# Kernel optimization log

Measured on AMD Instinct MI355X. Metric: run time of the kernel, lower is better.

Reference implementation:

```python
import jax, jax.numpy as jnp
import numpy as np

B, D, H = 32768, 256, 8
DH = D // H
SCALE = 1.0 / float(np.sqrt(DH))
# neighbor indices: for query node i, context = the other 3 nodes (in order)
NEIGH = np.array([[1, 2, 3], [0, 2, 3], [0, 1, 3], [0, 1, 2]], dtype=np.int32)


def setup_inputs() -> dict:
    key = jax.random.key(0)
    ks = jax.random.split(key, 6)
    s = 0.02
    mk = lambda k: jax.random.normal(k, (D, D), jnp.float32) * s
    return {
        "tokens": jax.random.normal(ks[0], (B, 4, D), jnp.float32),
        "Wq": mk(ks[1]),
        "Wk": mk(ks[2]),
        "Wv": mk(ks[3]),
        "Wr": mk(ks[4]),
        "Wo": mk(ks[5]),
        "ln_g": jnp.ones((D,), jnp.float32),
        "ln_b": jnp.zeros((D,), jnp.float32),
    }


def reference(tokens, Wq, Wk, Wv, Wr, Wo, ln_g, ln_b):
    # tokens: [B,4,D]. All 4 modality queries share one GCA block (share_gca=True),
    # so we batch the 4-node complete-graph message passing into one pass.
    neigh = jnp.asarray(NEIGH)
    ctx = tokens[:, neigh]                    # [B,4,3,D]
    Q = tokens @ Wq.T                         # [B,4,D]
    K = ctx @ Wk.T                            # [B,4,3,D]
    V = ctx @ Wv.T
    R = ctx @ Wr.T
    V_eff = jax.nn.sigmoid(R) * V             # gated values
    Qh = Q.reshape(B, 4, H, DH)
    Kh = K.reshape(B, 4, 3, H, DH)
    Vh = V_eff.reshape(B, 4, 3, H, DH)
    scores = jnp.einsum('bihd,bilhd->bihl', Qh, Kh) * SCALE   # [B,4,H,3]
    attn = jax.nn.softmax(scores, axis=-1)    # dropout = identity (eval mode)
    out = jnp.einsum('bihl,bilhd->bihd', attn, Vh).reshape(B, 4, D)
    out = out @ Wo.T
    y = tokens + out                          # residual
    mu = y.mean(-1, keepdims=True)
    var = y.var(-1, keepdims=True)
    y = (y - mu) / jnp.sqrt(var + 1e-5) * ln_g + ln_b   # LayerNorm
    # attn: [B,4,H,3] -> per-query attn maps (attn[:, i] == attn for modality-i query, [B,H,1,3] squeezed)
    return y, attn
```

## Files before the change

### kernel.cpp

```cpp
#include <hip/hip_runtime.h>
#include <stdint.h>


#define D_DIM   256
#define H_NUM   8
#define RT      64
#define NTHR    512
#define ROWS_TOT 131072
#define Y_SZ    33554432
#define SCALE_F 0.17677669529663687f
#define W_ELEMS 65536
#define WS_NEED (5 * W_ELEMS * 2)

#define SX_LD   264
#define AO_LD   264
#define SP_LD   20

typedef __attribute__((ext_vector_type(8))) short bf16x8;
typedef __attribute__((ext_vector_type(4))) float f32x4;

__device__ __forceinline__ float b2f(uint16_t s) {
    union { uint32_t u; float f; } c; c.u = ((uint32_t)s) << 16; return c.f;
}
__device__ __forceinline__ uint16_t f2b(float f) {
    union { float f; uint32_t u; } c; c.f = f;
    return (uint16_t)((c.u + 0x7fffu + ((c.u >> 16) & 1u)) >> 16);
}
__device__ __forceinline__ bf16x8 cvt8(const float* p) {
    const float4 a = *(const float4*)p;
    const float4 b = *(const float4*)(p + 4);
    bf16x8 r;
    r[0] = (short)f2b(a.x); r[1] = (short)f2b(a.y);
    r[2] = (short)f2b(a.z); r[3] = (short)f2b(a.w);
    r[4] = (short)f2b(b.x); r[5] = (short)f2b(b.y);
    r[6] = (short)f2b(b.z); r[7] = (short)f2b(b.w);
    return r;
}
__device__ __forceinline__ uint2 pack4(f32x4 a) {
    uint2 p;
    p.x = (uint32_t)f2b(a[0]) | ((uint32_t)f2b(a[1]) << 16);
    p.y = (uint32_t)f2b(a[2]) | ((uint32_t)f2b(a[3]) << 16);
    return p;
}

__global__ __launch_bounds__(256)
void conv_weights(const float* __restrict__ Wq, const float* __restrict__ Wk,
                  const float* __restrict__ Wv, const float* __restrict__ Wr,
                  const float* __restrict__ Wo, uint16_t* __restrict__ dst)
{
    const int m = blockIdx.x >> 6;
    const float* src = (m == 0) ? Wq : (m == 1) ? Wk : (m == 2) ? Wv
                     : (m == 3) ? Wr : Wo;
    const int base = (blockIdx.x & 63) * 1024 + threadIdx.x * 4;
    const float4 v = *(const float4*)&src[base];
    uint2 pk;
    pk.x = (uint32_t)f2b(v.x) | ((uint32_t)f2b(v.y) << 16);
    pk.y = (uint32_t)f2b(v.z) | ((uint32_t)f2b(v.w) << 16);
    *(uint2*)&dst[(size_t)m * W_ELEMS + base] = pk;
}

template<bool WBF16>
__global__ __launch_bounds__(NTHR, 4)
void cmaa_fused(const float* __restrict__ tok,
                const float* __restrict__ Wq, const float* __restrict__ Wk,
                const float* __restrict__ Wv, const float* __restrict__ Wr,
                const float* __restrict__ Wo,
                const uint16_t* __restrict__ wbf,
                const float* __restrict__ lng, const float* __restrict__ lnb,
                float* __restrict__ outp)
{
    __shared__ __align__(16) uint16_t sX [RT * SX_LD];
    __shared__ __align__(16) uint16_t sAO[RT * AO_LD];
    __shared__ __align__(16) uint16_t sAL[RT * H_NUM * 4];
    __shared__ __align__(16) float    sPT[RT * SP_LD];

    const int tid  = threadIdx.x;
    const int wv   = tid >> 6;
    const int lane = tid & 63;
    const int l15  = lane & 15;
    const int quad = lane >> 4;
    const int R0   = blockIdx.x * RT;

    {
        const float* g = tok + (size_t)R0 * D_DIM;
        #pragma unroll
        for (int it = 0; it < 4; ++it) {
            const int t = tid + it * NTHR;
            const int row = t >> 5, c = t & 31;
            *(bf16x8*)&sX[row * SX_LD + c * 8] = cvt8(&g[row * D_DIM + c * 8]);
        }
    }
    __syncthreads();

    const bool qk = (wv < 4);
    const int  hl = wv & 3;

    #pragma unroll
    for (int p = 0; p < 2; ++p) {
        const int h = p * 4 + hl;
        const int colbase = h * 32;
        const float*    WF0 = qk ? Wq : Wv;
        const float*    WF1 = qk ? Wk : Wr;
        const uint16_t* WB0 = wbf + (size_t)(qk ? 0 : 2) * W_ELEMS;
        const uint16_t* WB1 = WB0 + W_ELEMS;

        f32x4 acc[2][2][4];
        #pragma unroll
        for (int m = 0; m < 2; ++m)
            #pragma unroll
            for (int ct = 0; ct < 2; ++ct)
                #pragma unroll
                for (int nt = 0; nt < 4; ++nt)
                    acc[m][ct][nt] = (f32x4){0.f, 0.f, 0.f, 0.f};

        #pragma unroll
        for (int kk = 0; kk < 8; ++kk) {
            const int k0 = kk * 32;
            bf16x8 ax[4];
            #pragma unroll
            for (int nt = 0; nt < 4; ++nt)
                ax[nt] = *(const bf16x8*)&sX[(nt * 16 + l15) * SX_LD + k0 + quad * 8];
            bf16x8 b0[2], b1[2];
            #pragma unroll
            for (int ct = 0; ct < 2; ++ct) {
                const int wrow = colbase + ct * 16 + l15;
                if constexpr (WBF16) {
                    b0[ct] = *(const bf16x8*)&WB0[(size_t)wrow * D_DIM + k0 + quad * 8];
                    b1[ct] = *(const bf16x8*)&WB1[(size_t)wrow * D_DIM + k0 + quad * 8];
                } else {
                    b0[ct] = cvt8(&WF0[(size_t)wrow * D_DIM + k0 + quad * 8]);
                    b1[ct] = cvt8(&WF1[(size_t)wrow * D_DIM + k0 + quad * 8]);
                }
            }
            #pragma unroll
            for (int ct = 0; ct < 2; ++ct)
                #pragma unroll
                for (int nt = 0; nt < 4; ++nt)
                    acc[0][ct][nt] = __builtin_amdgcn_mfma_f32_16x16x32_bf16(b0[ct], ax[nt], acc[0][ct][nt], 0, 0, 0);
            #pragma unroll
            for (int ct = 0; ct < 2; ++ct)
                #pragma unroll
                for (int nt = 0; nt < 4; ++nt)
                    acc[1][ct][nt] = __builtin_amdgcn_mfma_f32_16x16x32_bf16(b1[ct], ax[nt], acc[1][ct][nt], 0, 0, 0);
        }

        if (qk) {
            #pragma unroll
            for (int nt = 0; nt < 4; ++nt) {
                float sc[3];
                #pragma unroll
                for (int m = 1; m <= 3; ++m) {
                    float s = 0.f;
                    #pragma unroll
                    for (int ct = 0; ct < 2; ++ct)
                        #pragma unroll
                        for (int r = 0; r < 4; ++r)
                            s += acc[0][ct][nt][r] * __shfl_xor(acc[1][ct][nt][r], m);
                    s += __shfl_xor(s, 16);
                    s += __shfl_xor(s, 32);
                    sc[m - 1] = s * SCALE_F;
                }
                const float mx = fmaxf(sc[0], fmaxf(sc[1], sc[2]));
                const float e1 = __expf(sc[0] - mx), e2 = __expf(sc[1] - mx), e3 = __expf(sc[2] - mx);
                const float inv = 1.f / (e1 + e2 + e3);
                const float a1 = e1 * inv, a2 = e2 * inv, a3 = e3 * inv;
                const int token = nt * 16 + l15;
                if (quad == 0) {
                    ushort4 aw;
                    aw.x = 0; aw.y = f2b(a1); aw.z = f2b(a2); aw.w = f2b(a3);
                    *(ushort4*)&sAL[(token * H_NUM + h) * 4] = aw;
                    const int ii = token & 3;
                    float* ap = outp + Y_SZ + ((size_t)(R0 + token) * H_NUM + h) * 3;
                    #pragma unroll
                    for (int l = 0; l < 3; ++l) {
                        const int jj = l + (l >= ii);
                        const int m  = ii ^ jj;
                        ap[l] = (m == 1) ? a1 : ((m == 2) ? a2 : a3);
                    }
                }
            }
        } else {
            #pragma unroll
            for (int ct = 0; ct < 2; ++ct)
                #pragma unroll
                for (int nt = 0; nt < 4; ++nt)
                    #pragma unroll
                    for (int r = 0; r < 4; ++r)
                        acc[0][ct][nt][r] *= 1.f / (1.f + __expf(-acc[1][ct][nt][r]));
        }
        __syncthreads();

        if (!qk) {
            #pragma unroll
            for (int nt = 0; nt < 4; ++nt) {
                const int token = nt * 16 + l15;
                const ushort4 aw = *(const ushort4*)&sAL[(token * H_NUM + h) * 4];
                const float a1 = b2f(aw.y), a2 = b2f(aw.z), a3 = b2f(aw.w);
                #pragma unroll
                for (int ct = 0; ct < 2; ++ct) {
                    f32x4 ao;
                    #pragma unroll
                    for (int r = 0; r < 4; ++r) {
                        const float v = acc[0][ct][nt][r];
                        ao[r] = a1 * __shfl_xor(v, 1)
                              + a2 * __shfl_xor(v, 2)
                              + a3 * __shfl_xor(v, 3);
                    }
                    *(uint2*)&sAO[token * AO_LD + colbase + ct * 16 + quad * 4] = pack4(ao);
                }
            }
        }
        __syncthreads();
    }

    const uint16_t* WoB = wbf + (size_t)4 * W_ELEMS;
    f32x4 acc3[2][4];
    #pragma unroll
    for (int ct = 0; ct < 2; ++ct)
        #pragma unroll
        for (int nt = 0; nt < 4; ++nt)
            acc3[ct][nt] = (f32x4){0.f, 0.f, 0.f, 0.f};

    #pragma unroll
    for (int kk = 0; kk < 8; ++kk) {
        const int k0 = kk * 32;
        bf16x8 ao[4];
        #pragma unroll
        for (int nt = 0; nt < 4; ++nt)
            ao[nt] = *(const bf16x8*)&sAO[(nt * 16 + l15) * AO_LD + k0 + quad * 8];
        bf16x8 bw[2];
        #pragma unroll
        for (int ct = 0; ct < 2; ++ct) {
            const int wrow = wv * 32 + ct * 16 + l15;
            if constexpr (WBF16)
                bw[ct] = *(const bf16x8*)&WoB[(size_t)wrow * D_DIM + k0 + quad * 8];
            else
                bw[ct] = cvt8(&Wo[(size_t)wrow * D_DIM + k0 + quad * 8]);
        }
        #pragma unroll
        for (int ct = 0; ct < 2; ++ct)
            #pragma unroll
            for (int nt = 0; nt < 4; ++nt)
                acc3[ct][nt] = __builtin_amdgcn_mfma_f32_16x16x32_bf16(bw[ct], ao[nt], acc3[ct][nt], 0, 0, 0);
    }

    #pragma unroll
    for (int nt = 0; nt < 4; ++nt) {
        const int token = nt * 16 + l15;
        float s1 = 0.f, s2 = 0.f;
        #pragma unroll
        for (int ct = 0; ct < 2; ++ct) {
            const ushort4 xv = *(const ushort4*)&sX[token * SX_LD + wv * 32 + ct * 16 + quad * 4];
            const float x0 = b2f(xv.x), x1 = b2f(xv.y), x2 = b2f(xv.z), x3 = b2f(xv.w);
            acc3[ct][nt][0] += x0; acc3[ct][nt][1] += x1;
            acc3[ct][nt][2] += x2; acc3[ct][nt][3] += x3;
            #pragma unroll
            for (int r = 0; r < 4; ++r) {
                const float y = acc3[ct][nt][r];
                s1 += y; s2 += y * y;
            }
        }
        s1 += __shfl_xor(s1, 16); s1 += __shfl_xor(s1, 32);
        s2 += __shfl_xor(s2, 16); s2 += __shfl_xor(s2, 32);
        if (quad == 0) {
            float2 ps; ps.x = s1; ps.y = s2;
            *(float2*)&sPT[token * SP_LD + wv * 2] = ps;
        }
    }
    __syncthreads();

    #pragma unroll
    for (int nt = 0; nt < 4; ++nt) {
        const int token = nt * 16 + l15;
        const f32x4* pp = (const f32x4*)&sPT[token * SP_LD];
        const f32x4 q0 = pp[0], q1 = pp[1], q2 = pp[2], q3 = pp[3];
        const float s1 = q0[0] + q0[2] + q1[0] + q1[2] + q2[0] + q2[2] + q3[0] + q3[2];
        const float s2 = q0[1] + q0[3] + q1[1] + q1[3] + q2[1] + q2[3] + q3[1] + q3[3];
        const float mean = s1 * (1.f / 256.f);
        const float var  = fmaxf(s2 * (1.f / 256.f) - mean * mean, 0.f);
        const float rstd = rsqrtf(var + 1e-5f);
        float* orow = outp + (size_t)(R0 + token) * D_DIM;
        #pragma unroll
        for (int ct = 0; ct < 2; ++ct) {
            const int c0 = wv * 32 + ct * 16 + quad * 4;
            const float4 g4 = *(const float4*)&lng[c0];
            const float4 b4 = *(const float4*)&lnb[c0];
            float4 o4;
            o4.x = (acc3[ct][nt][0] - mean) * rstd * g4.x + b4.x;
            o4.y = (acc3[ct][nt][1] - mean) * rstd * g4.y + b4.y;
            o4.z = (acc3[ct][nt][2] - mean) * rstd * g4.z + b4.z;
            o4.w = (acc3[ct][nt][3] - mean) * rstd * g4.w + b4.w;
            *(float4*)&orow[c0] = o4;
        }
    }
}

extern "C" void kernel_launch(void* const* d_in, const int* in_sizes, int n_in,
                              void* d_out, int out_size, void* d_ws, size_t ws_size,
                              hipStream_t stream) {
    (void)in_sizes; (void)n_in; (void)out_size;
    const float* tok = (const float*)d_in[0];
    const float* Wq  = (const float*)d_in[1];
    const float* Wk  = (const float*)d_in[2];
    const float* Wv  = (const float*)d_in[3];
    const float* Wr  = (const float*)d_in[4];
    const float* Wo  = (const float*)d_in[5];
    const float* lng = (const float*)d_in[6];
    const float* lnb = (const float*)d_in[7];
    float* outp = (float*)d_out;
    uint16_t* wbf = (uint16_t*)d_ws;

    dim3 grid(ROWS_TOT / RT), block(NTHR);
    if (ws_size >= (size_t)WS_NEED) {
        conv_weights<<<dim3(320), dim3(256), 0, stream>>>(Wq, Wk, Wv, Wr, Wo, wbf);
        cmaa_fused<true><<<grid, block, 0, stream>>>(
            tok, Wq, Wk, Wv, Wr, Wo, wbf, lng, lnb, outp);
    } else {
        cmaa_fused<false><<<grid, block, 0, stream>>>(
            tok, Wq, Wk, Wv, Wr, Wo, wbf, lng, lnb, outp);
    }
}
```

Baseline: 429.5 us.

## Preload weights into registers and stage attention maps in LDS for coalesced store

All weight fragments for each projection pass are loaded into registers before the MFMA loop, and the Wo fragments are prefetched during the second pass so their latency overlaps with the softmax and gating work. The attention probabilities are now kept in fp32 in shared memory in output order and written out as one coalesced float4 store per block, replacing scattered 4-byte global writes. The launch bound is lowered from 4 to 2 blocks per SM so the larger register footprint fits, which cuts occupancy.

```diff
diff --git a/kernel.cpp b/kernel.cpp
--- a/kernel.cpp
+++ b/kernel.cpp
@@ -60,7 +60,7 @@
 }
 
 template<bool WBF16>
-__global__ __launch_bounds__(NTHR, 4)
+__global__ __launch_bounds__(NTHR, 2)
 void cmaa_fused(const float* __restrict__ tok,
                 const float* __restrict__ Wq, const float* __restrict__ Wk,
                 const float* __restrict__ Wv, const float* __restrict__ Wr,
@@ -69,10 +69,10 @@
                 const float* __restrict__ lng, const float* __restrict__ lnb,
                 float* __restrict__ outp)
 {
-    __shared__ __align__(16) uint16_t sX [RT * SX_LD];
-    __shared__ __align__(16) uint16_t sAO[RT * AO_LD];
-    __shared__ __align__(16) uint16_t sAL[RT * H_NUM * 4];
-    __shared__ __align__(16) float    sPT[RT * SP_LD];
+    __shared__ __align__(16) uint16_t sX  [RT * SX_LD];
+    __shared__ __align__(16) uint16_t sAO [RT * AO_LD];
+    __shared__ __align__(16) float    sALf[RT * H_NUM * 3];
+    __shared__ __align__(16) float    sPT [RT * SP_LD];
 
     const int tid  = threadIdx.x;
     const int wv   = tid >> 6;
@@ -94,6 +94,8 @@
 
     const bool qk = (wv < 4);
     const int  hl = wv & 3;
+
+    bf16x8 wo_reg[2][8];
 
     #pragma unroll
     for (int p = 0; p < 2; ++p) {
@@ -104,6 +106,22 @@
         const uint16_t* WB0 = wbf + (size_t)(qk ? 0 : 2) * W_ELEMS;
         const uint16_t* WB1 = WB0 + W_ELEMS;
 
+        bf16x8 w0[2][8], w1[2][8];
+        #pragma unroll
+        for (int ct = 0; ct < 2; ++ct) {
+            const int wrow = colbase + ct * 16 + l15;
+            #pragma unroll
+            for (int kk = 0; kk < 8; ++kk) {
+                if constexpr (WBF16) {
+                    w0[ct][kk] = *(const bf16x8*)&WB0[(size_t)wrow * D_DIM + kk * 32 + quad * 8];
+                    w1[ct][kk] = *(const bf16x8*)&WB1[(size_t)wrow * D_DIM + kk * 32 + quad * 8];
+                } else {
+                    w0[ct][kk] = cvt8(&WF0[(size_t)wrow * D_DIM + kk * 32 + quad * 8]);
+                    w1[ct][kk] = cvt8(&WF1[(size_t)wrow * D_DIM + kk * 32 + quad * 8]);
+                }
+            }
+        }
+
         f32x4 acc[2][2][4];
         #pragma unroll
         for (int m = 0; m < 2; ++m)
@@ -120,28 +138,31 @@
             #pragma unroll
             for (int nt = 0; nt < 4; ++nt)
                 ax[nt] = *(const bf16x8*)&sX[(nt * 16 + l15) * SX_LD + k0 + quad * 8];
-            bf16x8 b0[2], b1[2];
+            #pragma unroll
+            for (int ct = 0; ct < 2; ++ct)
+                #pragma unroll
+                for (int nt = 0; nt < 4; ++nt)
+                    acc[0][ct][nt] = __builtin_amdgcn_mfma_f32_16x16x32_bf16(w0[ct][kk], ax[nt], acc[0][ct][nt], 0, 0, 0);
+            #pragma unroll
+            for (int ct = 0; ct < 2; ++ct)
+                #pragma unroll
+                for (int nt = 0; nt < 4; ++nt)
+                    acc[1][ct][nt] = __builtin_amdgcn_mfma_f32_16x16x32_bf16(w1[ct][kk], ax[nt], acc[1][ct][nt], 0, 0, 0);
+        }
+
+        if (p == 1) {
+            const uint16_t* WoB = wbf + (size_t)4 * W_ELEMS;
             #pragma unroll
             for (int ct = 0; ct < 2; ++ct) {
-                const int wrow = colbase + ct * 16 + l15;
-                if constexpr (WBF16) {
-                    b0[ct] = *(const bf16x8*)&WB0[(size_t)wrow * D_DIM + k0 + quad * 8];
-                    b1[ct] = *(const bf16x8*)&WB1[(size_t)wrow * D_DIM + k0 + quad * 8];
-                } else {
-                    b0[ct] = cvt8(&WF0[(size_t)wrow * D_DIM + k0 + quad * 8]);
-                    b1[ct] = cvt8(&WF1[(size_t)wrow * D_DIM + k0 + quad * 8]);
-                }
-            }
-            #pragma unroll
-            for (int ct = 0; ct < 2; ++ct)
-                #pragma unroll
-                for (int nt = 0; nt < 4; ++nt)
-                    acc[0][ct][nt] = __builtin_amdgcn_mfma_f32_16x16x32_bf16(b0[ct], ax[nt], acc[0][ct][nt], 0, 0, 0);
-            #pragma unroll
-            for (int ct = 0; ct < 2; ++ct)
-                #pragma unroll
-                for (int nt = 0; nt < 4; ++nt)
-                    acc[1][ct][nt] = __builtin_amdgcn_mfma_f32_16x16x32_bf16(b1[ct], ax[nt], acc[1][ct][nt], 0, 0, 0);
+                const int wrow = wv * 32 + ct * 16 + l15;
+                #pragma unroll
+                for (int kk = 0; kk < 8; ++kk) {
+                    if constexpr (WBF16)
+                        wo_reg[ct][kk] = *(const bf16x8*)&WoB[(size_t)wrow * D_DIM + kk * 32 + quad * 8];
+                    else
+                        wo_reg[ct][kk] = cvt8(&Wo[(size_t)wrow * D_DIM + kk * 32 + quad * 8]);
+                }
+            }
         }
 
         if (qk) {
@@ -163,19 +184,16 @@
                 const float mx = fmaxf(sc[0], fmaxf(sc[1], sc[2]));
                 const float e1 = __expf(sc[0] - mx), e2 = __expf(sc[1] - mx), e3 = __expf(sc[2] - mx);
                 const float inv = 1.f / (e1 + e2 + e3);
-                const float a1 = e1 * inv, a2 = e2 * inv, a3 = e3 * inv;
+                const float am[3] = { e1 * inv, e2 * inv, e3 * inv };
                 const int token = nt * 16 + l15;
                 if (quad == 0) {
-                    ushort4 aw;
-                    aw.x = 0; aw.y = f2b(a1); aw.z = f2b(a2); aw.w = f2b(a3);
-                    *(ushort4*)&sAL[(token * H_NUM + h) * 4] = aw;
                     const int ii = token & 3;
-                    float* ap = outp + Y_SZ + ((size_t)(R0 + token) * H_NUM + h) * 3;
+                    float* al = &sALf[(token * H_NUM + h) * 3];
                     #pragma unroll
                     for (int l = 0; l < 3; ++l) {
                         const int jj = l + (l >= ii);
                         const int m  = ii ^ jj;
-                        ap[l] = (m == 1) ? a1 : ((m == 2) ? a2 : a3);
+                        al[l] = am[m - 1];
                     }
                 }
             }
@@ -194,17 +212,24 @@
             #pragma unroll
             for (int nt = 0; nt < 4; ++nt) {
                 const int token = nt * 16 + l15;
-                const ushort4 aw = *(const ushort4*)&sAL[(token * H_NUM + h) * 4];
-                const float a1 = b2f(aw.y), a2 = b2f(aw.z), a3 = b2f(aw.w);
+                const int ii = token & 3;
+                const float* al = &sALf[(token * H_NUM + h) * 3];
+                float am[3];
+                #pragma unroll
+                for (int m = 1; m <= 3; ++m) {
+                    const int jj = ii ^ m;
+                    const int l  = jj - (jj > ii ? 1 : 0);
+                    am[m - 1] = al[l];
+                }
                 #pragma unroll
                 for (int ct = 0; ct < 2; ++ct) {
                     f32x4 ao;
                     #pragma unroll
                     for (int r = 0; r < 4; ++r) {
                         const float v = acc[0][ct][nt][r];
-                        ao[r] = a1 * __shfl_xor(v, 1)
-                              + a2 * __shfl_xor(v, 2)
-                              + a3 * __shfl_xor(v, 3);
+                        ao[r] = am[0] * __shfl_xor(v, 1)
+                              + am[1] * __shfl_xor(v, 2)
+                              + am[2] * __shfl_xor(v, 3);
                     }
                     *(uint2*)&sAO[token * AO_LD + colbase + ct * 16 + quad * 4] = pack4(ao);
                 }
@@ -213,7 +238,11 @@
         __syncthreads();
     }
 
-    const uint16_t* WoB = wbf + (size_t)4 * W_ELEMS;
+    if (tid < 384) {
+        const float4 v = *(const float4*)&sALf[tid * 4];
+        *(float4*)&outp[Y_SZ + (size_t)R0 * (H_NUM * 3) + tid * 4] = v;
+    }
+
     f32x4 acc3[2][4];
     #pragma unroll
     for (int ct = 0; ct < 2; ++ct)
@@ -228,20 +257,11 @@
         #pragma unroll
         for (int nt = 0; nt < 4; ++nt)
             ao[nt] = *(const bf16x8*)&sAO[(nt * 16 + l15) * AO_LD + k0 + quad * 8];
-        bf16x8 bw[2];
-        #pragma unroll
-        for (int ct = 0; ct < 2; ++ct) {
-            const int wrow = wv * 32 + ct * 16 + l15;
-            if constexpr (WBF16)
-                bw[ct] = *(const bf16x8*)&WoB[(size_t)wrow * D_DIM + k0 + quad * 8];
-            else
-                bw[ct] = cvt8(&Wo[(size_t)wrow * D_DIM + k0 + quad * 8]);
-        }
         #pragma unroll
         for (int ct = 0; ct < 2; ++ct)
             #pragma unroll
             for (int nt = 0; nt < 4; ++nt)
-                acc3[ct][nt] = __builtin_amdgcn_mfma_f32_16x16x32_bf16(bw[ct], ao[nt], acc3[ct][nt], 0, 0, 0);
+                acc3[ct][nt] = __builtin_amdgcn_mfma_f32_16x16x32_bf16(wo_reg[ct][kk], ao[nt], acc3[ct][nt], 0, 0, 0);
     }
 
     #pragma unroll
```

Result: slower. 452.1 us (+5.3%).

## Use 1024-thread blocks and MFMA for attention scores and weighted values

Applied to the files above, without the earlier changes.

Doubles the block to 16 waves so Q/K and V/R projections all run in one pass, one head per wave, instead of two passes over 8 waves. Q and K are staged to shared memory and the gated V is stored transposed. The per-token 4x4 score matrix and the attention-weighted sum of V are then computed with small MFMA ops instead of cross-lane shuffles. The attention maps are written out as coalesced float4 stores from shared memory. In exchange, shared memory per block and per-thread register pressure rise, occupancy may drop, and the small MFMAs are mostly zero-padded.

```diff
diff --git a/kernel.cpp b/kernel.cpp
--- a/kernel.cpp
+++ b/kernel.cpp
@@ -5,7 +5,7 @@
 #define D_DIM   256
 #define H_NUM   8
 #define RT      64
-#define NTHR    512
+#define NTHR    1024
 #define ROWS_TOT 131072
 #define Y_SZ    33554432
 #define SCALE_F 0.17677669529663687f
@@ -13,8 +13,9 @@
 #define WS_NEED (5 * W_ELEMS * 2)
 
 #define SX_LD   264
-#define AO_LD   264
-#define SP_LD   20
+#define QK_LD   264
+#define VT_LD   68
+#define SP_LD   36
 
 typedef __attribute__((ext_vector_type(8))) short bf16x8;
 typedef __attribute__((ext_vector_type(4))) float f32x4;
@@ -69,10 +70,13 @@
                 const float* __restrict__ lng, const float* __restrict__ lnb,
                 float* __restrict__ outp)
 {
-    __shared__ __align__(16) uint16_t sX [RT * SX_LD];
-    __shared__ __align__(16) uint16_t sAO[RT * AO_LD];
-    __shared__ __align__(16) uint16_t sAL[RT * H_NUM * 4];
-    __shared__ __align__(16) float    sPT[RT * SP_LD];
+    __shared__ __align__(16) uint16_t sX  [RT * SX_LD];
+    __shared__ __align__(16) uint16_t sQ  [RT * QK_LD];
+    __shared__ __align__(16) uint16_t sK  [RT * QK_LD];
+    __shared__ __align__(16) uint16_t sVT [D_DIM * VT_LD];
+    __shared__ __align__(16) float    sALf[RT * H_NUM * 3];
+    __shared__ __align__(16) uint2    sALpk[RT * H_NUM];
+    __shared__ __align__(16) float    sPT [RT * SP_LD];
 
     const int tid  = threadIdx.x;
     const int wv   = tid >> 6;
@@ -84,7 +88,7 @@
     {
         const float* g = tok + (size_t)R0 * D_DIM;
         #pragma unroll
-        for (int it = 0; it < 4; ++it) {
+        for (int it = 0; it < 2; ++it) {
             const int t = tid + it * NTHR;
             const int row = t >> 5, c = t & 31;
             *(bf16x8*)&sX[row * SX_LD + c * 8] = cvt8(&g[row * D_DIM + c * 8]);
@@ -92,16 +96,12 @@
     }
     __syncthreads();
 
-    const bool qk = (wv < 4);
-    const int  hl = wv & 3;
-
-    #pragma unroll
-    for (int p = 0; p < 2; ++p) {
-        const int h = p * 4 + hl;
-        const int colbase = h * 32;
-        const float*    WF0 = qk ? Wq : Wv;
-        const float*    WF1 = qk ? Wk : Wr;
-        const uint16_t* WB0 = wbf + (size_t)(qk ? 0 : 2) * W_ELEMS;
+    {
+        const bool qkw = (wv < 8);
+        const int  h   = wv & 7;
+        const float*    WF0 = qkw ? Wq : Wv;
+        const float*    WF1 = qkw ? Wk : Wr;
+        const uint16_t* WB0 = wbf + (size_t)(qkw ? 0 : 2) * W_ELEMS;
         const uint16_t* WB1 = WB0 + W_ELEMS;
 
         f32x4 acc[2][2][4];
@@ -123,7 +123,7 @@
             bf16x8 b0[2], b1[2];
             #pragma unroll
             for (int ct = 0; ct < 2; ++ct) {
-                const int wrow = colbase + ct * 16 + l15;
+                const int wrow = h * 32 + ct * 16 + l15;
                 if constexpr (WBF16) {
                     b0[ct] = *(const bf16x8*)&WB0[(size_t)wrow * D_DIM + k0 + quad * 8];
                     b1[ct] = *(const bf16x8*)&WB1[(size_t)wrow * D_DIM + k0 + quad * 8];
@@ -144,154 +144,172 @@
                     acc[1][ct][nt] = __builtin_amdgcn_mfma_f32_16x16x32_bf16(b1[ct], ax[nt], acc[1][ct][nt], 0, 0, 0);
         }
 
-        if (qk) {
-            #pragma unroll
-            for (int nt = 0; nt < 4; ++nt) {
-                float sc[3];
-                #pragma unroll
-                for (int m = 1; m <= 3; ++m) {
-                    float s = 0.f;
-                    #pragma unroll
-                    for (int ct = 0; ct < 2; ++ct)
-                        #pragma unroll
-                        for (int r = 0; r < 4; ++r)
-                            s += acc[0][ct][nt][r] * __shfl_xor(acc[1][ct][nt][r], m);
-                    s += __shfl_xor(s, 16);
-                    s += __shfl_xor(s, 32);
-                    sc[m - 1] = s * SCALE_F;
+        if (qkw) {
+            #pragma unroll
+            for (int ct = 0; ct < 2; ++ct)
+                #pragma unroll
+                for (int nt = 0; nt < 4; ++nt) {
+                    const int tk = nt * 16 + l15;
+                    const int dc = h * 32 + ct * 16 + quad * 4;
+                    *(uint2*)&sQ[tk * QK_LD + dc] = pack4(acc[0][ct][nt]);
+                    *(uint2*)&sK[tk * QK_LD + dc] = pack4(acc[1][ct][nt]);
                 }
-                const float mx = fmaxf(sc[0], fmaxf(sc[1], sc[2]));
-                const float e1 = __expf(sc[0] - mx), e2 = __expf(sc[1] - mx), e3 = __expf(sc[2] - mx);
-                const float inv = 1.f / (e1 + e2 + e3);
-                const float a1 = e1 * inv, a2 = e2 * inv, a3 = e3 * inv;
-                const int token = nt * 16 + l15;
-                if (quad == 0) {
-                    ushort4 aw;
-                    aw.x = 0; aw.y = f2b(a1); aw.z = f2b(a2); aw.w = f2b(a3);
-                    *(ushort4*)&sAL[(token * H_NUM + h) * 4] = aw;
-                    const int ii = token & 3;
-                    float* ap = outp + Y_SZ + ((size_t)(R0 + token) * H_NUM + h) * 3;
-                    #pragma unroll
-                    for (int l = 0; l < 3; ++l) {
-                        const int jj = l + (l >= ii);
-                        const int m  = ii ^ jj;
-                        ap[l] = (m == 1) ? a1 : ((m == 2) ? a2 : a3);
-                    }
-                }
-            }
         } else {
             #pragma unroll
             for (int ct = 0; ct < 2; ++ct)
                 #pragma unroll
                 for (int nt = 0; nt < 4; ++nt)
                     #pragma unroll
-                    for (int r = 0; r < 4; ++r)
-                        acc[0][ct][nt][r] *= 1.f / (1.f + __expf(-acc[1][ct][nt][r]));
-        }
-        __syncthreads();
-
-        if (!qk) {
-            #pragma unroll
-            for (int nt = 0; nt < 4; ++nt) {
-                const int token = nt * 16 + l15;
-                const ushort4 aw = *(const ushort4*)&sAL[(token * H_NUM + h) * 4];
-                const float a1 = b2f(aw.y), a2 = b2f(aw.z), a3 = b2f(aw.w);
-                #pragma unroll
-                for (int ct = 0; ct < 2; ++ct) {
-                    f32x4 ao;
-                    #pragma unroll
                     for (int r = 0; r < 4; ++r) {
-                        const float v = acc[0][ct][nt][r];
-                        ao[r] = a1 * __shfl_xor(v, 1)
-                              + a2 * __shfl_xor(v, 2)
-                              + a3 * __shfl_xor(v, 3);
+                        const float ve = acc[0][ct][nt][r] *
+                            (1.f / (1.f + __expf(-acc[1][ct][nt][r])));
+                        const int dd = h * 32 + ct * 16 + quad * 4 + r;
+                        sVT[dd * VT_LD + nt * 16 + l15] = f2b(ve);
                     }
-                    *(uint2*)&sAO[token * AO_LD + colbase + ct * 16 + quad * 4] = pack4(ao);
-                }
+        }
+    }
+    __syncthreads();
+
+    #pragma unroll
+    for (int uu = 0; uu < 2; ++uu) {
+        const int u  = wv + 16 * uu;
+        const int hh = u >> 2;
+        const int tt = u & 3;
+        const int tk = tt * 16 + l15;
+
+        const bf16x8 kf = *(const bf16x8*)&sK[tk * QK_LD + hh * 32 + quad * 8];
+        const bf16x8 qf = *(const bf16x8*)&sQ[tk * QK_LD + hh * 32 + quad * 8];
+        f32x4 sc = __builtin_amdgcn_mfma_f32_16x16x32_bf16(
+            kf, qf, (f32x4){0.f, 0.f, 0.f, 0.f}, 0, 0, 0);
+
+        if (quad == (l15 >> 2)) {
+            const int r0 = l15 & 3;
+            float sv[4], e[4];
+            #pragma unroll
+            for (int r = 0; r < 4; ++r) sv[r] = sc[r] * SCALE_F;
+            float mx = -1e30f;
+            #pragma unroll
+            for (int r = 0; r < 4; ++r) mx = fmaxf(mx, (r == r0) ? -1e30f : sv[r]);
+            float sum = 0.f;
+            #pragma unroll
+            for (int r = 0; r < 4; ++r) {
+                e[r] = (r == r0) ? 0.f : __expf(sv[r] - mx);
+                sum += e[r];
             }
-        }
-        __syncthreads();
-    }
-
-    const uint16_t* WoB = wbf + (size_t)4 * W_ELEMS;
-    f32x4 acc3[2][4];
+            const float inv = 1.f / sum;
+            float al[4];
+            #pragma unroll
+            for (int r = 0; r < 4; ++r) al[r] = e[r] * inv;
+            float* af = &sALf[(tk * H_NUM + hh) * 3];
+            #pragma unroll
+            for (int r = 0; r < 4; ++r)
+                if (r != r0) af[r - (r > r0 ? 1 : 0)] = al[r];
+            uint2 pk;
+            pk.x = (uint32_t)f2b(al[0]) | ((uint32_t)f2b(al[1]) << 16);
+            pk.y = (uint32_t)f2b(al[2]) | ((uint32_t)f2b(al[3]) << 16);
+            sALpk[tk * H_NUM + hh] = pk;
+        }
+
+        const uint2 apk = sALpk[tk * H_NUM + hh];
+        const bool qm = (quad == ((l15 >> 3) & 1));
+        const bool hi = (l15 & 4) != 0;
+        union { uint32_t u[4]; bf16x8 v; } A;
+        A.u[0] = (qm && !hi) ? apk.x : 0u;
+        A.u[1] = (qm && !hi) ? apk.y : 0u;
+        A.u[2] = (qm &&  hi) ? apk.x : 0u;
+        A.u[3] = (qm &&  hi) ? apk.y : 0u;
+
+        const bf16x8 vb0 = *(const bf16x8*)&sVT[(hh * 32 + l15) * VT_LD + tt * 16 + quad * 8];
+        const bf16x8 vb1 = *(const bf16x8*)&sVT[(hh * 32 + 16 + l15) * VT_LD + tt * 16 + quad * 8];
+        const f32x4 ao0 = __builtin_amdgcn_mfma_f32_16x16x32_bf16(
+            A.v, vb0, (f32x4){0.f, 0.f, 0.f, 0.f}, 0, 0, 0);
+        const f32x4 ao1 = __builtin_amdgcn_mfma_f32_16x16x32_bf16(
+            A.v, vb1, (f32x4){0.f, 0.f, 0.f, 0.f}, 0, 0, 0);
+
+        #pragma unroll
+        for (int r = 0; r < 4; ++r) {
+            const int tw = tt * 16 + quad * 4 + r;
+            sQ[tw * QK_LD + hh * 32 + l15]      = f2b(ao0[r]);
+            sQ[tw * QK_LD + hh * 32 + 16 + l15] = f2b(ao1[r]);
+        }
+    }
+    __syncthreads();
+
+    if (tid < 384) {
+        const float4 v = *(const float4*)&sALf[tid * 4];
+        *(float4*)&outp[Y_SZ + (size_t)R0 * 24 + tid * 4] = v;
+    }
+
+    f32x4 acc3[4];
     #pragma unroll
-    for (int ct = 0; ct < 2; ++ct)
-        #pragma unroll
-        for (int nt = 0; nt < 4; ++nt)
-            acc3[ct][nt] = (f32x4){0.f, 0.f, 0.f, 0.f};
-
-    #pragma unroll
-    for (int kk = 0; kk < 8; ++kk) {
-        const int k0 = kk * 32;
-        bf16x8 ao[4];
-        #pragma unroll
-        for (int nt = 0; nt < 4; ++nt)
-            ao[nt] = *(const bf16x8*)&sAO[(nt * 16 + l15) * AO_LD + k0 + quad * 8];
-        bf16x8 bw[2];
-        #pragma unroll
-        for (int ct = 0; ct < 2; ++ct) {
-            const int wrow = wv * 32 + ct * 16 + l15;
+    for (int nt = 0; nt < 4; ++nt) acc3[nt] = (f32x4){0.f, 0.f, 0.f, 0.f};
+
+    {
+        const uint16_t* WoB = wbf + (size_t)4 * W_ELEMS;
+        #pragma unroll
+        for (int kk = 0; kk < 8; ++kk) {
+            const int k0 = kk * 32;
+            bf16x8 ao[4];
+            #pragma unroll
+            for (int nt = 0; nt < 4; ++nt)
+                ao[nt] = *(const bf16x8*)&sQ[(nt * 16 + l15) * QK_LD + k0 + quad * 8];
+            bf16x8 wo;
+            const int wrow = wv * 16 + l15;
             if constexpr (WBF16)
-                bw[ct] = *(const bf16x8*)&WoB[(size_t)wrow * D_DIM + k0 + quad * 8];
+                wo = *(const bf16x8*)&WoB[(size_t)wrow * D_DIM + k0 + quad * 8];
             else
-                bw[ct] = cvt8(&Wo[(size_t)wrow * D_DIM + k0 + quad * 8]);
-        }
-        #pragma unroll
-        for (int ct = 0; ct < 2; ++ct)
+                wo = cvt8(&Wo[(size_t)wrow * D_DIM + k0 + quad * 8]);
             #pragma unroll
             for (int nt = 0; nt < 4; ++nt)
-                acc3[ct][nt] = __builtin_amdgcn_mfma_f32_16x16x32_bf16(bw[ct], ao[nt], acc3[ct][nt], 0, 0, 0);
+                acc3[nt] = __builtin_amdgcn_mfma_f32_16x16x32_bf16(wo, ao[nt], acc3[nt], 0, 0, 0);
+        }
     }
 
     #pragma unroll
     for (int nt = 0; nt < 4; ++nt) {
-        const int token = nt * 16 + l15;
+        const int tk = nt * 16 + l15;
+        const ushort4 xv = *(const ushort4*)&sX[tk * SX_LD + wv * 16 + quad * 4];
+        acc3[nt][0] += b2f(xv.x); acc3[nt][1] += b2f(xv.y);
+        acc3[nt][2] += b2f(xv.z); acc3[nt][3] += b2f(xv.w);
         float s1 = 0.f, s2 = 0.f;
         #pragma unroll
-        for (int ct = 0; ct < 2; ++ct) {
-            const ushort4 xv = *(const ushort4*)&sX[token * SX_LD + wv * 32 + ct * 16 + quad * 4];
-            const float x0 = b2f(xv.x), x1 = b2f(xv.y), x2 = b2f(xv.z), x3 = b2f(xv.w);
-            acc3[ct][nt][0] += x0; acc3[ct][nt][1] += x1;
-            acc3[ct][nt][2] += x2; acc3[ct][nt][3] += x3;
-            #pragma unroll
-            for (int r = 0; r < 4; ++r) {
-                const float y = acc3[ct][nt][r];
-                s1 += y; s2 += y * y;
-            }
+        for (int r = 0; r < 4; ++r) {
+            const float y = acc3[nt][r];
+            s1 += y; s2 += y * y;
         }
         s1 += __shfl_xor(s1, 16); s1 += __shfl_xor(s1, 32);
         s2 += __shfl_xor(s2, 16); s2 += __shfl_xor(s2, 32);
         if (quad == 0) {
             float2 ps; ps.x = s1; ps.y = s2;
-            *(float2*)&sPT[token * SP_LD + wv * 2] = ps;
+            *(float2*)&sPT[tk * SP_LD + wv * 2] = ps;
         }
     }
     __syncthreads();
 
     #pragma unroll
     for (int nt = 0; nt < 4; ++nt) {
-        const int token = nt * 16 + l15;
-        const f32x4* pp = (const f32x4*)&sPT[token * SP_LD];
-        const f32x4 q0 = pp[0], q1 = pp[1], q2 = pp[2], q3 = pp[3];
-        const float s1 = q0[0] + q0[2] + q1[0] + q1[2] + q2[0] + q2[2] + q3[0] + q3[2];
-        const float s2 = q0[1] + q0[3] + q1[1] + q1[3] + q2[1] + q2[3] + q3[1] + q3[3];
+        const int tk = nt * 16 + l15;
+        const f32x4* pp = (const f32x4*)&sPT[tk * SP_LD];
+        float s1 = 0.f, s2 = 0.f;
+        #pragma unroll
+        for (int j = 0; j < 8; ++j) {
+            const f32x4 q = pp[j];
+            s1 += q[0] + q[2];
+            s2 += q[1] + q[3];
+        }
         const float mean = s1 * (1.f / 256.f);
         const float var  = fmaxf(s2 * (1.f / 256.f) - mean * mean, 0.f);
         const float rstd = rsqrtf(var + 1e-5f);
-        float* orow = outp + (size_t)(R0 + token) * D_DIM;
-        #pragma unroll
-        for (int ct = 0; ct < 2; ++ct) {
-            const int c0 = wv * 32 + ct * 16 + quad * 4;
-            const float4 g4 = *(const float4*)&lng[c0];
-            const float4 b4 = *(const float4*)&lnb[c0];
-            float4 o4;
-            o4.x = (acc3[ct][nt][0] - mean) * rstd * g4.x + b4.x;
-            o4.y = (acc3[ct][nt][1] - mean) * rstd * g4.y + b4.y;
-            o4.z = (acc3[ct][nt][2] - mean) * rstd * g4.z + b4.z;
-            o4.w = (acc3[ct][nt][3] - mean) * rstd * g4.w + b4.w;
-            *(float4*)&orow[c0] = o4;
-        }
+        float* orow = outp + (size_t)(R0 + tk) * D_DIM;
+        const int c0 = wv * 16 + quad * 4;
+        const float4 g4 = *(const float4*)&lng[c0];
+        const float4 b4 = *(const float4*)&lnb[c0];
+        float4 o4;
+        o4.x = (acc3[nt][0] - mean) * rstd * g4.x + b4.x;
+        o4.y = (acc3[nt][1] - mean) * rstd * g4.y + b4.y;
+        o4.z = (acc3[nt][2] - mean) * rstd * g4.z + b4.z;
+        o4.w = (acc3[nt][3] - mean) * rstd * g4.w + b4.w;
+        *(float4*)&orow[c0] = o4;
     }
 }
 
```

Measured after the change: 444.2 us. 3.4% more time.
